# Kernel optimization log

Measured on AMD Instinct MI355X. Metric: run time of the kernel, lower is better.

## Reference

```python
import jax, jax.numpy as jnp
import numpy as np


def setup_inputs() -> dict:
    key = jax.random.key(0)
    k1, k2, k3, k4 = jax.random.split(key, 4)
    c = 256
    x = jax.random.normal(k1, (4, c, 64, 64), dtype=jnp.float32)
    # 1x1 conv weights act as channel-mixing matrices
    w_qkv = jax.random.normal(k2, (3 * c, c), dtype=jnp.float32) * (1.0 / np.sqrt(c))
    w_out = jax.random.normal(k3, (c, c), dtype=jnp.float32) * (1.0 / np.sqrt(c))
    b_out = jax.random.normal(k4, (c,), dtype=jnp.float32) * 0.01
    return {"x": x, "w_qkv": w_qkv, "w_out": w_out, "b_out": b_out}


def reference(x, w_qkv, w_out, b_out):
    b, c, h, w = x.shape
    heads = 4
    d = c // heads
    scale = d ** (-0.5)
    hw = h * w

    # 1x1 conv (no bias): [b,3c,h,w]
    qkv = jnp.einsum('oc,bchw->bohw', w_qkv, x)
    q, k, v = jnp.split(qkv, 3, axis=1)

    def to_seq(t):
        # [b,c,h,w] -> [b,heads,hw,d]
        return t.reshape(b, heads, d, hw).transpose(0, 1, 3, 2)

    q, k, v = to_seq(q), to_seq(k), to_seq(v)

    sim = jnp.einsum('bhid,bhjd->bhij', q, k) * scale
    attn = jax.nn.softmax(sim, axis=-1)
    out = jnp.einsum('bhij,bhjd->bhid', attn, v)

    # [b,heads,hw,d] -> [b,c,h,w]
    out = out.transpose(0, 1, 3, 2).reshape(b, c, h, w)

    # output 1x1 conv with bias, plus residual
    proj = jnp.einsum('oc,bchw->bohw', w_out, out) + b_out[None, :, None, None]
    return x + proj
```

## Files before the change

### kernel.cpp

```cpp
#include <hip/hip_runtime.h>


#define HW 4096
#define CIN 256
#define LOG2E_DIV8 0.18033688011112042f

typedef __attribute__((ext_vector_type(8))) short short8v;
typedef __attribute__((ext_vector_type(4))) short short4v;
typedef __attribute__((ext_vector_type(4))) float float4v;
typedef __attribute__((ext_vector_type(16))) float f32x16;
typedef __attribute__((ext_vector_type(4))) unsigned int uint4v;

static __device__ __forceinline__ unsigned short f2bf(float f) {
    unsigned int u = __float_as_uint(f);
    u += 0x7fff + ((u >> 16) & 1);
    return (unsigned short)(u >> 16);
}
static __device__ __forceinline__ unsigned int pkbf(float a, float b) {
    unsigned int r;
    asm("v_cvt_pk_bf16_f32 %0, %1, %2" : "=v"(r) : "v"(a), "v"(b));
    return r;
}
static __device__ __forceinline__ void pl32swap(unsigned int& a, unsigned int& b) {
    asm volatile("v_permlane32_swap_b32 %0, %1" : "+v"(a), "+v"(b));
}
static __device__ __forceinline__ float fmax3(float a, float b, float c) {
    return fmaxf(fmaxf(a, b), c);
}

__global__ __launch_bounds__(256) void cast_w_k(
    const float* __restrict__ w_qkv, const float* __restrict__ w_out,
    unsigned short* __restrict__ wqb, unsigned short* __restrict__ wob)
{
    const int bi = blockIdx.x;
    if (bi < 192) {
        const int idx = bi * 1024 + threadIdx.x * 4;
        const float s = (idx < 256 * 256) ? LOG2E_DIV8 : 1.0f;
        const float4 v = *(const float4*)&w_qkv[idx];
        uint2 pk;
        pk.x = pkbf(v.x * s, v.y * s);
        pk.y = pkbf(v.z * s, v.w * s);
        *(uint2*)&wqb[idx] = pk;
    } else {
        const int idx = (bi - 192) * 1024 + threadIdx.x * 4;
        const float4 v = *(const float4*)&w_out[idx];
        uint2 pk;
        pk.x = pkbf(v.x, v.y);
        pk.y = pkbf(v.z, v.w);
        *(uint2*)&wob[idx] = pk;
    }
}

__global__ __launch_bounds__(256) void cast_x_k(
    const float* __restrict__ x, unsigned short* __restrict__ xt)
{
    const int p0 = blockIdx.x * 64, c0 = blockIdx.y * 64, b = blockIdx.z;
    const int t = threadIdx.x;
    __shared__ float tile[64][65];

    const float* xb = x + ((size_t)b * CIN + c0) * HW + p0;
    #pragma unroll
    for (int iter = 0; iter < 4; ++iter) {
        const int idx = iter * 1024 + t * 4;
        const int cc = idx >> 6, pp = idx & 63;
        const float4 v = *(const float4*)&xb[(size_t)cc * HW + pp];
        tile[cc][pp + 0] = v.x; tile[cc][pp + 1] = v.y;
        tile[cc][pp + 2] = v.z; tile[cc][pp + 3] = v.w;
    }
    __syncthreads();
    unsigned short* xo = xt + ((size_t)b * HW + p0) * CIN + c0;
    #pragma unroll
    for (int iter = 0; iter < 4; ++iter) {
        const int idx = iter * 1024 + t * 4;
        const int pp = idx >> 6, cc = idx & 63;
        uint2 pk;
        pk.x = pkbf(tile[cc + 0][pp], tile[cc + 1][pp]);
        pk.y = pkbf(tile[cc + 2][pp], tile[cc + 3][pp]);
        *(uint2*)&xo[(size_t)pp * CIN + cc] = pk;
    }
}

__global__ __launch_bounds__(256) void qkv_mfma_k(
    const unsigned short* __restrict__ wqb, const unsigned short* __restrict__ xt,
    unsigned short* __restrict__ qb, unsigned short* __restrict__ kb,
    unsigned short* __restrict__ vb)
{
    const int o0 = blockIdx.x * 128;
    const int p0 = blockIdx.y * 128;
    const int b  = blockIdx.z;
    const int t = threadIdx.x;
    const int wid = t >> 6, lane = t & 63, g = lane >> 4, li = lane & 15;
    const int wo = (wid >> 1) * 64, wp = (wid & 1) * 64;

    __shared__ char alds[16384];
    __shared__ char blds[16384];

    const int srow8 = t >> 3, sc16 = t & 7;
    const char* asrc = (const char*)wqb + ((size_t)(o0 + srow8) * 256) * 2 + sc16 * 16;
    const char* bsrc = (const char*)xt + (((size_t)b * HW + p0 + srow8) * 256) * 2 + sc16 * 16;

    float4 areg[4], breg[4];
    #pragma unroll
    for (int it = 0; it < 4; ++it) {
        areg[it] = *(const float4*)(asrc + (size_t)it * 32 * 512);
        breg[it] = *(const float4*)(bsrc + (size_t)it * 32 * 512);
    }

    float4v acc[4][4];
    #pragma unroll
    for (int mt = 0; mt < 4; ++mt)
        #pragma unroll
        for (int nt = 0; nt < 4; ++nt) acc[mt][nt] = (float4v){0.f, 0.f, 0.f, 0.f};

    for (int ks = 0; ks < 4; ++ks) {
        #pragma unroll
        for (int it = 0; it < 4; ++it) {
            const int row = it * 32 + srow8;
            const int dsw = row * 128 + ((sc16 * 16) ^ ((row & 7) << 4));
            *(float4*)(alds + dsw) = areg[it];
            *(float4*)(blds + dsw) = breg[it];
        }
        __syncthreads();
        if (ks < 3) {
            #pragma unroll
            for (int it = 0; it < 4; ++it) {
                areg[it] = *(const float4*)(asrc + (size_t)it * 32 * 512 + (ks + 1) * 128);
                breg[it] = *(const float4*)(bsrc + (size_t)it * 32 * 512 + (ks + 1) * 128);
            }
        }
        short8v af[4][2], bf[4][2];
        #pragma unroll
        for (int mt = 0; mt < 4; ++mt) {
            const int row = wo + mt * 16 + li;
            #pragma unroll
            for (int kc = 0; kc < 2; ++kc)
                af[mt][kc] = *(const short8v*)(alds + row * 128 + ((kc * 64 + g * 16) ^ ((row & 7) << 4)));
        }
        #pragma unroll
        for (int nt = 0; nt < 4; ++nt) {
            const int row = wp + nt * 16 + li;
            #pragma unroll
            for (int kc = 0; kc < 2; ++kc)
                bf[nt][kc] = *(const short8v*)(blds + row * 128 + ((kc * 64 + g * 16) ^ ((row & 7) << 4)));
        }
        #pragma unroll
        for (int mt = 0; mt < 4; ++mt)
            #pragma unroll
            for (int nt = 0; nt < 4; ++nt) {
                acc[mt][nt] = __builtin_amdgcn_mfma_f32_16x16x32_bf16(af[mt][0], bf[nt][0], acc[mt][nt], 0, 0, 0);
                acc[mt][nt] = __builtin_amdgcn_mfma_f32_16x16x32_bf16(af[mt][1], bf[nt][1], acc[mt][nt], 0, 0, 0);
            }
        __syncthreads();
    }

    const int which = o0 >> 8;
    #pragma unroll
    for (int mt = 0; mt < 4; ++mt) {
        const int o_b = o0 + wo + mt * 16 + g * 4;
        const int head = (o_b >> 6) & 3;
        const int dd = o_b & 63;
        const int bh = b * 4 + head;
        if (which < 2) {
            unsigned short* dst = which ? kb : qb;
            #pragma unroll
            for (int nt = 0; nt < 4; ++nt) {
                const int p = p0 + wp + nt * 16 + li;
                uint2 pk;
                pk.x = pkbf(acc[mt][nt][0], acc[mt][nt][1]);
                pk.y = pkbf(acc[mt][nt][2], acc[mt][nt][3]);
                *(uint2*)&dst[((size_t)bh * HW + p) * 64 + dd] = pk;
            }
        } else {
            #pragma unroll
            for (int nt = 0; nt < 4; ++nt) {
                const int p = p0 + wp + nt * 16 + li;
                #pragma unroll
                for (int r = 0; r < 4; ++r)
                    vb[((size_t)bh * 64 + dd + r) * HW + p] = f2bf(acc[mt][nt][r]);
            }
        }
    }
}

__global__ __launch_bounds__(512, 2) void flash_mfma_k(
    const unsigned short* __restrict__ qb, const unsigned short* __restrict__ kb,
    const unsigned short* __restrict__ vb, unsigned short* __restrict__ att)
{
    const int i0 = blockIdx.x * 128;
    const int bh = blockIdx.y;
    const int t = threadIdx.x;
    const int wid = t >> 6, lane = t & 63;
    const int q32 = lane & 31, hi = lane >> 5;
    const int sp = t >> 8;
    const int w4 = wid & 3;
    const int b = bh >> 2, head = bh & 3;

    const unsigned short* qg = qb + (size_t)bh * HW * 64;
    const unsigned short* kg = kb + (size_t)bh * HW * 64 + (size_t)sp * 2048 * 64;
    const unsigned short* vg = vb + (size_t)bh * 64 * HW + (size_t)sp * 2048;

    __shared__ char smem[65536];
    char* const kls = smem + sp * 16384;
    char* const vls = smem + 32768 + sp * 16384;

    const int q = i0 + w4 * 32 + q32;
    short8v qf[4];
    #pragma unroll
    for (int kc = 0; kc < 4; ++kc)
        qf[kc] = *(const short8v*)(qg + (size_t)q * 64 + kc * 16 + hi * 8);

    short8v ones;
    #pragma unroll
    for (int i = 0; i < 8; ++i) ones[i] = (short)0x3F80;

    float m = 0.f;
    f32x16 acco[2];
    f32x16 accl;
    f32x16 accs[2];
    short8v pf[2][2];
    #pragma unroll
    for (int r = 0; r < 16; ++r) { acco[0][r] = 0.f; acco[1][r] = 0.f; accl[r] = 0.f; }

    const int ts = t & 255;
    const int srow0 = ts >> 3, sc0 = ts & 7;
    const int srow1 = srow0 + 32;
    const int dsw0 = srow0 * 128 + ((sc0 * 16) ^ ((srow0 & 7) << 4));
    const int dsw1 = srow1 * 128 + ((sc0 * 16) ^ ((srow1 & 7) << 4));
    const char* ksrc0 = (const char*)kg + (size_t)srow0 * 128 + sc0 * 16;
    const char* ksrc1 = (const char*)kg + (size_t)srow1 * 128 + sc0 * 16;
    const char* vsrc0 = (const char*)vg + (size_t)srow0 * 8192 + sc0 * 16;
    const char* vsrc1 = (const char*)vg + (size_t)srow1 * 8192 + sc0 * 16;

    float4 kregA, kregB, vregA, vregB;

    auto LOADT = [&](int tile) {
        kregA = *(const float4*)(ksrc0 + (size_t)tile * 8192);
        kregB = *(const float4*)(ksrc1 + (size_t)tile * 8192);
        vregA = *(const float4*)(vsrc0 + (size_t)tile * 128);
        vregB = *(const float4*)(vsrc1 + (size_t)tile * 128);
    };
    auto WRITET = [&](int buf) {
        *(float4*)(kls + buf * 8192 + dsw0) = kregA;
        *(float4*)(kls + buf * 8192 + dsw1) = kregB;
        *(float4*)(vls + buf * 8192 + dsw0) = vregA;
        *(float4*)(vls + buf * 8192 + dsw1) = vregB;
    };
    auto SMM = [&](int buf) {
        #pragma unroll
        for (int r = 0; r < 16; ++r) { accs[0][r] = -m; accs[1][r] = -m; }
        __builtin_amdgcn_s_setprio(1);
        #pragma unroll
        for (int jt = 0; jt < 2; ++jt) {
            const int row = jt * 32 + q32;
            const char* kbase = kls + buf * 8192 + row * 128;
            const int sw = (row & 7) << 4;
            #pragma unroll
            for (int kc = 0; kc < 4; ++kc) {
                const short8v kf = *(const short8v*)(kbase + ((kc * 32 + hi * 16) ^ sw));
                accs[jt] = __builtin_amdgcn_mfma_f32_32x32x16_bf16(kf, qf[kc], accs[jt], 0, 0, 0);
            }
        }
        __builtin_amdgcn_s_setprio(0);
    };
    auto SOFT = [&]() {
        float mx[16];
        #pragma unroll
        for (int r = 0; r < 16; ++r) mx[r] = fmaxf(accs[0][r], accs[1][r]);
        float a0 = fmax3(mx[0],  mx[1],  mx[2]);
        float a1 = fmax3(mx[3],  mx[4],  mx[5]);
        float a2 = fmax3(mx[6],  mx[7],  mx[8]);
        float a3 = fmax3(mx[9],  mx[10], mx[11]);
        float a4 = fmax3(mx[12], mx[13], mx[14]);
        float b0 = fmax3(a0, a1, a2);
        float b1 = fmax3(a3, a4, mx[15]);
        float tm = fmaxf(b0, b1);
        tm = fmaxf(tm, __shfl_xor(tm, 32, 64));
        if (__any(tm > 8.0f)) {
            const float delta = fmaxf(tm, 0.f);
            const float fsc = __builtin_amdgcn_exp2f(-delta);
            m += delta;
            accl[0] *= fsc;
            #pragma unroll
            for (int r = 0; r < 16; ++r) { acco[0][r] *= fsc; acco[1][r] *= fsc; }
            #pragma unroll
            for (int r = 0; r < 16; ++r) { accs[0][r] -= delta; accs[1][r] -= delta; }
        }
        #pragma unroll
        for (int jt = 0; jt < 2; ++jt) {
            float p[16];
            #pragma unroll
            for (int r = 0; r < 16; ++r) p[r] = __builtin_amdgcn_exp2f(accs[jt][r]);
            unsigned int w0 = pkbf(p[0], p[1]);
            unsigned int w1 = pkbf(p[2], p[3]);
            unsigned int w2 = pkbf(p[4], p[5]);
            unsigned int w3 = pkbf(p[6], p[7]);
            pl32swap(w0, w2);
            pl32swap(w1, w3);
            uint4v fa; fa[0] = w0; fa[1] = w1; fa[2] = w2; fa[3] = w3;
            pf[jt][0] = __builtin_bit_cast(short8v, fa);
            unsigned int w4_ = pkbf(p[8],  p[9]);
            unsigned int w5 = pkbf(p[10], p[11]);
            unsigned int w6 = pkbf(p[12], p[13]);
            unsigned int w7 = pkbf(p[14], p[15]);
            pl32swap(w4_, w6);
            pl32swap(w5, w7);
            uint4v fb; fb[0] = w4_; fb[1] = w5; fb[2] = w6; fb[3] = w7;
            pf[jt][1] = __builtin_bit_cast(short8v, fb);
        }
    };
    auto PVMM = [&](int buf) {
        __builtin_amdgcn_s_setprio(1);
        #pragma unroll
        for (int jt = 0; jt < 2; ++jt)
            #pragma unroll
            for (int kr = 0; kr < 2; ++kr)
                accl = __builtin_amdgcn_mfma_f32_32x32x16_bf16(ones, pf[jt][kr], accl, 0, 0, 0);
        #pragma unroll
        for (int dt = 0; dt < 2; ++dt) {
            const int row = dt * 32 + q32;
            const char* vbase = vls + buf * 8192 + row * 128;
            const int sw = (row & 7) << 4;
            #pragma unroll
            for (int jt = 0; jt < 2; ++jt)
                #pragma unroll
                for (int kr = 0; kr < 2; ++kr) {
                    const short8v vf = *(const short8v*)(vbase + ((jt * 64 + kr * 32 + hi * 16) ^ sw));
                    acco[dt] = __builtin_amdgcn_mfma_f32_32x32x16_bf16(vf, pf[jt][kr], acco[dt], 0, 0, 0);
                }
        }
        __builtin_amdgcn_s_setprio(0);
    };

    LOADT(0);
    WRITET(0);
    LOADT(1);
    __syncthreads();
    SMM(0);

    for (int kt = 0; kt < 31; ++kt) {
        const int nb = (kt + 1) & 1;
        WRITET(nb);
        const int pref = (kt + 2 < 32) ? kt + 2 : 31;
        LOADT(pref);
        SOFT();
        PVMM(kt & 1);
        __syncthreads();
        SMM(nb);
    }
    SOFT();
    PVMM(1);

    __syncthreads();
    float* ex  = (float*)smem;
    float* mlx = (float*)(smem + 32768);
    if (sp == 1) {
        #pragma unroll
        for (int dt = 0; dt < 2; ++dt)
            #pragma unroll
            for (int r = 0; r < 16; ++r) {
                const int d = dt * 32 + 8 * (r >> 2) + 4 * hi + (r & 3);
                ex[w4 * 2048 + d * 32 + q32] = acco[dt][r];
            }
        if (hi == 0) {
            mlx[(w4 * 32 + q32) * 2 + 0] = m;
            mlx[(w4 * 32 + q32) * 2 + 1] = accl[0];
        }
    }
    __syncthreads();
    if (sp == 0) {
        const float m1 = mlx[(w4 * 32 + q32) * 2 + 0];
        const float l1 = mlx[(w4 * 32 + q32) * 2 + 1];
        const float mxm = fmaxf(m, m1);
        float f0 = __builtin_amdgcn_exp2f(m - mxm);
        float f1 = __builtin_amdgcn_exp2f(m1 - mxm);
        const float inv = 1.0f / (accl[0] * f0 + l1 * f1);
        f0 *= inv; f1 *= inv;
        unsigned short* ao = att + ((size_t)b * HW + q) * CIN + head * 64;
        #pragma unroll
        for (int dt = 0; dt < 2; ++dt)
            #pragma unroll
            for (int g4 = 0; g4 < 4; ++g4) {
                const int d0 = dt * 32 + 8 * g4 + 4 * hi;
                const float* exb = ex + w4 * 2048 + d0 * 32 + q32;
                const float v0 = acco[dt][g4 * 4 + 0] * f0 + exb[0]  * f1;
                const float v1 = acco[dt][g4 * 4 + 1] * f0 + exb[32] * f1;
                const float v2 = acco[dt][g4 * 4 + 2] * f0 + exb[64] * f1;
                const float v3 = acco[dt][g4 * 4 + 3] * f0 + exb[96] * f1;
                uint2 pk;
                pk.x = pkbf(v0, v1);
                pk.y = pkbf(v2, v3);
                *(uint2*)&ao[d0] = pk;
            }
    }
}

__global__ __launch_bounds__(256) void proj_mfma_k(
    const unsigned short* __restrict__ wob, const unsigned short* __restrict__ att,
    const float* __restrict__ bias, const float* __restrict__ x,
    float* __restrict__ out)
{
    const int o0 = blockIdx.x * 128;
    const int p0 = blockIdx.y * 128;
    const int b  = blockIdx.z;
    const int t = threadIdx.x;
    const int wid = t >> 6, lane = t & 63, g = lane >> 4, li = lane & 15;
    const int wo = (wid >> 1) * 64, wp = (wid & 1) * 64;

    __shared__ char alds[16384];
    __shared__ char blds[16384];

    const int srow8 = t >> 3, sc16 = t & 7;
    const char* asrc = (const char*)wob + ((size_t)(o0 + srow8) * 256) * 2 + sc16 * 16;
    const char* bsrc = (const char*)att + (((size_t)b * HW + p0 + srow8) * 256) * 2 + sc16 * 16;

    float4 areg[4], breg[4];
    #pragma unroll
    for (int it = 0; it < 4; ++it) {
        areg[it] = *(const float4*)(asrc + (size_t)it * 32 * 512);
        breg[it] = *(const float4*)(bsrc + (size_t)it * 32 * 512);
    }

    float4v acc[4][4];
    #pragma unroll
    for (int mt = 0; mt < 4; ++mt)
        #pragma unroll
        for (int nt = 0; nt < 4; ++nt) acc[mt][nt] = (float4v){0.f, 0.f, 0.f, 0.f};

    for (int ks = 0; ks < 4; ++ks) {
        #pragma unroll
        for (int it = 0; it < 4; ++it) {
            const int row = it * 32 + srow8;
            const int dsw = row * 128 + ((sc16 * 16) ^ ((row & 7) << 4));
            *(float4*)(alds + dsw) = areg[it];
            *(float4*)(blds + dsw) = breg[it];
        }
        __syncthreads();
        if (ks < 3) {
            #pragma unroll
            for (int it = 0; it < 4; ++it) {
                areg[it] = *(const float4*)(asrc + (size_t)it * 32 * 512 + (ks + 1) * 128);
                breg[it] = *(const float4*)(bsrc + (size_t)it * 32 * 512 + (ks + 1) * 128);
            }
        }
        short8v af[4][2], bf[4][2];
        #pragma unroll
        for (int mt = 0; mt < 4; ++mt) {
            const int row = wo + mt * 16 + li;
            #pragma unroll
            for (int kc = 0; kc < 2; ++kc)
                af[mt][kc] = *(const short8v*)(alds + row * 128 + ((kc * 64 + g * 16) ^ ((row & 7) << 4)));
        }
        #pragma unroll
        for (int nt = 0; nt < 4; ++nt) {
            const int row = wp + nt * 16 + li;
            #pragma unroll
            for (int kc = 0; kc < 2; ++kc)
                bf[nt][kc] = *(const short8v*)(blds + row * 128 + ((kc * 64 + g * 16) ^ ((row & 7) << 4)));
        }
        #pragma unroll
        for (int mt = 0; mt < 4; ++mt)
            #pragma unroll
            for (int nt = 0; nt < 4; ++nt) {
                acc[mt][nt] = __builtin_amdgcn_mfma_f32_16x16x32_bf16(af[mt][0], bf[nt][0], acc[mt][nt], 0, 0, 0);
                acc[mt][nt] = __builtin_amdgcn_mfma_f32_16x16x32_bf16(af[mt][1], bf[nt][1], acc[mt][nt], 0, 0, 0);
            }
        __syncthreads();
    }

    #pragma unroll
    for (int mt = 0; mt < 4; ++mt) {
        const int o_b = o0 + wo + mt * 16 + g * 4;
        #pragma unroll
        for (int nt = 0; nt < 4; ++nt) {
            const int p = p0 + wp + nt * 16 + li;
            #pragma unroll
            for (int r = 0; r < 4; ++r) {
                const int o = o_b + r;
                const size_t ix = ((size_t)b * CIN + o) * HW + p;
                out[ix] = acc[mt][nt][r] + bias[o] + x[ix];
            }
        }
    }
}

extern "C" void kernel_launch(void* const* d_in, const int* in_sizes, int n_in,
                              void* d_out, int out_size, void* d_ws, size_t ws_size,
                              hipStream_t stream)
{
    const float* x     = (const float*)d_in[0];
    const float* w_qkv = (const float*)d_in[1];
    const float* w_out = (const float*)d_in[2];
    const float* b_out = (const float*)d_in[3];
    float* out = (float*)d_out;

    char* ws = (char*)d_ws;
    const size_t MB = 1024 * 1024;
    unsigned short* xt  = (unsigned short*)(ws);
    unsigned short* qb  = (unsigned short*)(ws + 8 * MB);
    unsigned short* kb  = (unsigned short*)(ws + 16 * MB);
    unsigned short* vb  = (unsigned short*)(ws + 24 * MB);
    unsigned short* att = (unsigned short*)(ws + 32 * MB);
    unsigned short* wqb = (unsigned short*)(ws + 40 * MB);
    unsigned short* wob = (unsigned short*)(ws + 40 * MB + 768 * 256 * 2);

    cast_w_k<<<256, 256, 0, stream>>>(w_qkv, w_out, wqb, wob);
    cast_x_k<<<dim3(64, 4, 4), 256, 0, stream>>>(x, xt);
    qkv_mfma_k<<<dim3(6, 32, 4), 256, 0, stream>>>(wqb, xt, qb, kb, vb);
    flash_mfma_k<<<dim3(32, 16), 512, 0, stream>>>(qb, kb, vb, att);
    proj_mfma_k<<<dim3(2, 32, 4), 256, 0, stream>>>(wob, att, b_out, x, out);
}
```

Measured before the change: 160.6 us.

## Stream K/V tiles directly into LDS and compute row sums on VALU

Staging of K/V tiles through registers (global load, then LDS store) is replaced with direct global-to-LDS async loads (global_load_lds). The XOR swizzle moves to the global source address, and the loop issues the next tile before computing on the current one. The softmax denominator is now summed with VALU adds and a cross-half shuffle, instead of extra MFMAs against a vector of ones. This trims MFMA work per tile and frees staging registers, but relies on the barrier waiting for outstanding async loads to be correct.

Result: faster. 149.2 us (-7.1%).

```diff
diff --git a/kernel.cpp b/kernel.cpp
--- a/kernel.cpp
+++ b/kernel.cpp
@@ -10,6 +10,9 @@
 typedef __attribute__((ext_vector_type(4))) float float4v;
 typedef __attribute__((ext_vector_type(16))) float f32x16;
 typedef __attribute__((ext_vector_type(4))) unsigned int uint4v;
+
+typedef const __attribute__((address_space(1))) unsigned int* gptr_t;
+typedef __attribute__((address_space(3))) unsigned int* lptr_t;
 
 static __device__ __forceinline__ unsigned short f2bf(float f) {
     unsigned int u = __float_as_uint(f);
@@ -209,41 +212,36 @@
     for (int kc = 0; kc < 4; ++kc)
         qf[kc] = *(const short8v*)(qg + (size_t)q * 64 + kc * 16 + hi * 8);
 
-    short8v ones;
-    #pragma unroll
-    for (int i = 0; i < 8; ++i) ones[i] = (short)0x3F80;
-
     float m = 0.f;
+    float l = 0.f;
     f32x16 acco[2];
-    f32x16 accl;
     f32x16 accs[2];
     short8v pf[2][2];
     #pragma unroll
-    for (int r = 0; r < 16; ++r) { acco[0][r] = 0.f; acco[1][r] = 0.f; accl[r] = 0.f; }
+    for (int r = 0; r < 16; ++r) { acco[0][r] = 0.f; acco[1][r] = 0.f; }
 
     const int ts = t & 255;
-    const int srow0 = ts >> 3, sc0 = ts & 7;
-    const int srow1 = srow0 + 32;
-    const int dsw0 = srow0 * 128 + ((sc0 * 16) ^ ((srow0 & 7) << 4));
-    const int dsw1 = srow1 * 128 + ((sc0 * 16) ^ ((srow1 & 7) << 4));
-    const char* ksrc0 = (const char*)kg + (size_t)srow0 * 128 + sc0 * 16;
-    const char* ksrc1 = (const char*)kg + (size_t)srow1 * 128 + sc0 * 16;
-    const char* vsrc0 = (const char*)vg + (size_t)srow0 * 8192 + sc0 * 16;
-    const char* vsrc1 = (const char*)vg + (size_t)srow1 * 8192 + sc0 * 16;
-
-    float4 kregA, kregB, vregA, vregB;
-
-    auto LOADT = [&](int tile) {
-        kregA = *(const float4*)(ksrc0 + (size_t)tile * 8192);
-        kregB = *(const float4*)(ksrc1 + (size_t)tile * 8192);
-        vregA = *(const float4*)(vsrc0 + (size_t)tile * 128);
-        vregB = *(const float4*)(vsrc1 + (size_t)tile * 128);
-    };
-    auto WRITET = [&](int buf) {
-        *(float4*)(kls + buf * 8192 + dsw0) = kregA;
-        *(float4*)(kls + buf * 8192 + dsw1) = kregB;
-        *(float4*)(vls + buf * 8192 + dsw0) = vregA;
-        *(float4*)(vls + buf * 8192 + dsw1) = vregB;
+    const int srow = ts >> 3;
+    const int scol = (ts & 7) * 16;
+    const int ssw  = (srow & 7) << 4;
+    const char* kgsrc0 = (const char*)kg + (size_t)srow * 128 + (scol ^ ssw);
+    const char* kgsrc1 = kgsrc0 + 32 * 128;
+    const char* vgsrc0 = (const char*)vg + (size_t)srow * 8192 + (scol ^ ssw);
+    const char* vgsrc1 = vgsrc0 + (size_t)32 * 8192;
+
+    auto ISSUE = [&](int tile, int buf) {
+        __builtin_amdgcn_global_load_lds(
+            (gptr_t)(kgsrc0 + (size_t)tile * 8192),
+            (lptr_t)(kls + buf * 8192 + ts * 16), 16, 0, 0);
+        __builtin_amdgcn_global_load_lds(
+            (gptr_t)(kgsrc1 + (size_t)tile * 8192),
+            (lptr_t)(kls + buf * 8192 + 4096 + ts * 16), 16, 0, 0);
+        __builtin_amdgcn_global_load_lds(
+            (gptr_t)(vgsrc0 + (size_t)tile * 128),
+            (lptr_t)(vls + buf * 8192 + ts * 16), 16, 0, 0);
+        __builtin_amdgcn_global_load_lds(
+            (gptr_t)(vgsrc1 + (size_t)tile * 128),
+            (lptr_t)(vls + buf * 8192 + 4096 + ts * 16), 16, 0, 0);
     };
     auto SMM = [&](int buf) {
         #pragma unroll
@@ -279,17 +277,23 @@
             const float delta = fmaxf(tm, 0.f);
             const float fsc = __builtin_amdgcn_exp2f(-delta);
             m += delta;
-            accl[0] *= fsc;
+            l *= fsc;
             #pragma unroll
             for (int r = 0; r < 16; ++r) { acco[0][r] *= fsc; acco[1][r] *= fsc; }
             #pragma unroll
             for (int r = 0; r < 16; ++r) { accs[0][r] -= delta; accs[1][r] -= delta; }
         }
+        float ls = 0.f;
         #pragma unroll
         for (int jt = 0; jt < 2; ++jt) {
             float p[16];
             #pragma unroll
             for (int r = 0; r < 16; ++r) p[r] = __builtin_amdgcn_exp2f(accs[jt][r]);
+            float s0 = (p[0] + p[1]) + (p[2] + p[3]);
+            float s1 = (p[4] + p[5]) + (p[6] + p[7]);
+            float s2 = (p[8] + p[9]) + (p[10] + p[11]);
+            float s3 = (p[12] + p[13]) + (p[14] + p[15]);
+            ls += (s0 + s1) + (s2 + s3);
             unsigned int w0 = pkbf(p[0], p[1]);
             unsigned int w1 = pkbf(p[2], p[3]);
             unsigned int w2 = pkbf(p[4], p[5]);
@@ -307,14 +311,10 @@
             uint4v fb; fb[0] = w4_; fb[1] = w5; fb[2] = w6; fb[3] = w7;
             pf[jt][1] = __builtin_bit_cast(short8v, fb);
         }
+        l += ls;
     };
     auto PVMM = [&](int buf) {
         __builtin_amdgcn_s_setprio(1);
-        #pragma unroll
-        for (int jt = 0; jt < 2; ++jt)
-            #pragma unroll
-            for (int kr = 0; kr < 2; ++kr)
-                accl = __builtin_amdgcn_mfma_f32_32x32x16_bf16(ones, pf[jt][kr], accl, 0, 0, 0);
         #pragma unroll
         for (int dt = 0; dt < 2; ++dt) {
             const int row = dt * 32 + q32;
@@ -331,28 +331,22 @@
         __builtin_amdgcn_s_setprio(0);
     };
 
-    LOADT(0);
-    WRITET(0);
-    LOADT(1);
+    ISSUE(0, 0);
     __syncthreads();
-    SMM(0);
-
-    for (int kt = 0; kt < 31; ++kt) {
-        const int nb = (kt + 1) & 1;
-        WRITET(nb);
-        const int pref = (kt + 2 < 32) ? kt + 2 : 31;
-        LOADT(pref);
+
+    int buf = 0;
+    for (int kt = 0; kt < 32; ++kt) {
+        if (kt < 31) ISSUE(kt + 1, buf ^ 1);
+        SMM(buf);
         SOFT();
-        PVMM(kt & 1);
+        PVMM(buf);
         __syncthreads();
-        SMM(nb);
-    }
-    SOFT();
-    PVMM(1);
-
-    __syncthreads();
+        buf ^= 1;
+    }
+
     float* ex  = (float*)smem;
     float* mlx = (float*)(smem + 32768);
+    const float ltot = l + __shfl_xor(l, 32, 64);
     if (sp == 1) {
         #pragma unroll
         for (int dt = 0; dt < 2; ++dt)
@@ -363,7 +357,7 @@
             }
         if (hi == 0) {
             mlx[(w4 * 32 + q32) * 2 + 0] = m;
-            mlx[(w4 * 32 + q32) * 2 + 1] = accl[0];
+            mlx[(w4 * 32 + q32) * 2 + 1] = ltot;
         }
     }
     __syncthreads();
@@ -373,7 +367,7 @@
         const float mxm = fmaxf(m, m1);
         float f0 = __builtin_amdgcn_exp2f(m - mxm);
         float f1 = __builtin_amdgcn_exp2f(m1 - mxm);
-        const float inv = 1.0f / (accl[0] * f0 + l1 * f1);
+        const float inv = 1.0f / (ltot * f0 + l1 * f1);
         f0 *= inv; f1 *= inv;
         unsigned short* ao = att + ((size_t)b * HW + q) * CIN + head * 64;
         #pragma unroll
```
